# Optimization experiments

Measured on AMD Instinct MI355X. Metric: run time of the kernel, lower is better.

The kernel has to match this reference:

```python
import jax, jax.numpy as jnp
import numpy as np

EMBED_DIM = 384
NUM_HEADS = 6
HEAD_DIM = EMBED_DIM // NUM_HEADS
SCALE = HEAD_DIM ** (-0.5)
B, T, N = 8, 64, 196


def setup_inputs() -> dict:
    key = jax.random.key(0)
    k1, k2, k3, k4, k5 = jax.random.split(key, 5)
    x = jax.random.normal(k1, (B, T, N, EMBED_DIM), dtype=jnp.float32)
    W_qkv = jax.random.normal(k2, (3 * EMBED_DIM, EMBED_DIM), dtype=jnp.float32) * 0.02
    b_qkv = jax.random.normal(k3, (3 * EMBED_DIM,), dtype=jnp.float32) * 0.02
    W_proj = jax.random.normal(k4, (EMBED_DIM, EMBED_DIM), dtype=jnp.float32) * 0.02
    b_proj = jax.random.normal(k5, (EMBED_DIM,), dtype=jnp.float32) * 0.02
    return {"x": x, "W_qkv": W_qkv, "b_qkv": b_qkv, "W_proj": W_proj, "b_proj": b_proj}


def reference(x, W_qkv, b_qkv, W_proj, b_proj):
    b, t, n, c = x.shape
    # qkv projection: [B,T,N,3C] -> [B,T,N,3,H,hd] -> [3,B,H,T,N,hd]
    qkv = jnp.einsum('btnc,oc->btno', x, W_qkv) + b_qkv
    qkv = qkv.reshape(b, t, n, 3, NUM_HEADS, HEAD_DIM)
    qkv = jnp.transpose(qkv, (3, 0, 4, 1, 2, 5))
    q, k, v = qkv[0], qkv[1], qkv[2]
    q = q * SCALE
    # scores over patches within each block: [B,H,T,N,N]
    attn = jnp.einsum('bhtnd,bhtmd->bhtnm', q, k)
    attn = jax.nn.softmax(attn, axis=-1)
    out = jnp.einsum('bhtnm,bhtmd->bhtnd', attn, v)  # [B,H,T,N,hd]
    # Faithful to original: permute(0,2,3,4,1) puts head_dim before head, then flatten
    out = jnp.transpose(out, (0, 2, 3, 4, 1)).reshape(b, t, n, c)
    out = jnp.einsum('btnc,oc->btno', out, W_proj) + b_proj
    return out
```

## Files before the change

### kernel.cpp

```cpp
#include <hip/hip_runtime.h>
#include <cstdint>
#include <cstddef>

typedef unsigned short u16;
typedef __attribute__((ext_vector_type(4))) float f32x4;
typedef __attribute__((ext_vector_type(8))) __bf16 bf16x8;
typedef __attribute__((ext_vector_type(8))) unsigned short u16x8;
typedef __attribute__((ext_vector_type(4))) unsigned short u16x4;

#define M_TOTAL 100352
#define K_DIM   384
#define QKV_N   1152
#define NHEADS  6
#define NPAT    196
#define SCL     0.125f

__device__ __forceinline__ u16 f2bf(float f) {
    unsigned int u = __builtin_bit_cast(unsigned int, f);
    u += 0x7fffu + ((u >> 16) & 1u);
    return (u16)(u >> 16);
}

__device__ __forceinline__ void gload16(const void* g, void* l) {
    __builtin_amdgcn_global_load_lds(
        (const __attribute__((address_space(1))) unsigned int*)g,
        (__attribute__((address_space(3))) unsigned int*)l, 16, 0, 0);
}

__device__ __forceinline__ int xcd_swz(int bid, int per_xcd) {
    return (bid & 7) * per_xcd + (bid >> 3);
}

__global__ void cvt_bf16_kern(const float* __restrict__ in, u16* __restrict__ out, int n8) {
    int i = blockIdx.x * 256 + threadIdx.x;
    if (i >= n8) return;
    const float4* p = (const float4*)in + (size_t)i * 2;
    float4 a = p[0], b = p[1];
    u16x8 o;
    o[0]=f2bf(a.x); o[1]=f2bf(a.y); o[2]=f2bf(a.z); o[3]=f2bf(a.w);
    o[4]=f2bf(b.x); o[5]=f2bf(b.y); o[6]=f2bf(b.z); o[7]=f2bf(b.w);
    *((u16x8*)out + i) = o;
}

__global__ void cvt_wproj_kern(const float* __restrict__ in, u16* __restrict__ out) {
    int i = blockIdx.x * 256 + threadIdx.x;
    int o = i / 384;
    int c = i - o * 384;
    int d = c & 63, h = c >> 6;
    out[i] = f2bf(in[(size_t)o * 384 + d * 6 + h]);
}

template<int NOUT, bool BF16OUT, bool QSCALE>
__global__ __launch_bounds__(256, 2) void gemm_kern(
        const u16* __restrict__ A, const u16* __restrict__ Bw,
        const float* __restrict__ bias, void* __restrict__ outp) {
    constexpr int NB = NOUT / 128;
    constexpr int PER_XCD = (M_TOTAL / 128) * NB / 8;
    __shared__ u16 As[128 * 64];
    __shared__ u16 Bs[128 * 64];
    int wg = xcd_swz(blockIdx.x, PER_XCD);
    int bm = wg / NB, bn = wg % NB;
    int tid = threadIdx.x;
    int l = tid & 63, w = tid >> 6;
    int wr = w >> 1, wc = w & 1;
    f32x4 acc[4][4] = {};
    const u16* Ag = A + (size_t)bm * 128 * K_DIM;
    const u16* Bg = Bw + (size_t)bn * 128 * K_DIM;

    for (int ks = 0; ks < 6; ++ks) {
#pragma unroll
        for (int i = 0; i < 4; ++i) {
            int c = i * 256 + tid;
            int row = c >> 3, cc = c & 7;
            int scc = cc ^ (row & 7);
            gload16(Ag + (size_t)row * K_DIM + ks * 64 + scc * 8, (u16*)As + c * 8);
            gload16(Bg + (size_t)row * K_DIM + ks * 64 + scc * 8, (u16*)Bs + c * 8);
        }
        __syncthreads();
#pragma unroll
        for (int kk = 0; kk < 2; ++kk) {
            bf16x8 af[4], bfr[4];
            int ccr = kk * 4 + (l >> 4);
#pragma unroll
            for (int m = 0; m < 4; ++m) {
                int ar = wr * 64 + m * 16 + (l & 15);
                af[m] = *(const bf16x8*)&As[ar * 64 + ((ccr ^ (ar & 7)) << 3)];
            }
#pragma unroll
            for (int n = 0; n < 4; ++n) {
                int br = wc * 64 + n * 16 + (l & 15);
                bfr[n] = *(const bf16x8*)&Bs[br * 64 + ((ccr ^ (br & 7)) << 3)];
            }
#pragma unroll
            for (int m = 0; m < 4; ++m)
#pragma unroll
                for (int n = 0; n < 4; ++n)
                    acc[m][n] = __builtin_amdgcn_mfma_f32_16x16x32_bf16(af[m], bfr[n], acc[m][n], 0, 0, 0);
        }
        __syncthreads();
    }
#pragma unroll
    for (int n = 0; n < 4; ++n) {
        int col = bn * 128 + wc * 64 + n * 16 + (l & 15);
        float bv = bias[col];
#pragma unroll
        for (int m = 0; m < 4; ++m) {
            int row0 = bm * 128 + wr * 64 + m * 16 + (l >> 4) * 4;
#pragma unroll
            for (int r = 0; r < 4; ++r) {
                float v = acc[m][n][r] + bv;
                if constexpr (QSCALE) { if (col < 384) v *= SCL; }
                if constexpr (BF16OUT)
                    ((u16*)outp)[(size_t)(row0 + r) * NOUT + col] = f2bf(v);
                else
                    ((float*)outp)[(size_t)(row0 + r) * NOUT + col] = v;
            }
        }
    }
}

__global__ __launch_bounds__(256, 2) void attn_kern(const u16* __restrict__ qkv,
                                                    u16* __restrict__ osc) {
    __shared__ u16 k_lds[208 * 72];
    __shared__ u16 vT[64 * 232];
    __shared__ u16 p_lds[4 * 16 * 36];

    int wg = xcd_swz(blockIdx.x, 384);
    int h = wg % NHEADS;
    int bt = wg / NHEADS;
    size_t m_base = (size_t)bt * NPAT;
    int tid = threadIdx.x, l = tid & 63, w = tid >> 6;

    {
        int d0 = (tid & 7) * 8;
#pragma unroll
        for (int it = 0; it < 7; ++it) {
            int n = it * 32 + (tid >> 3);
            if (n < 208) {
                u16x8 val = {};
                if (n < 196)
                    val = *(const u16x8*)(qkv + (m_base + n) * QKV_N + 384 + h * 64 + d0);
                *(u16x8*)&k_lds[n * 72 + d0] = val;
            }
        }
    }
    {
        int d0 = w * 16;
#pragma unroll
        for (int it = 0; it < 4; ++it) {
            int n = it * 64 + l;
            if (n < 232) {
                u16x8 v0 = {}, v1 = {};
                if (n < 196) {
                    const u16* src = qkv + (m_base + n) * QKV_N + 768 + h * 64 + d0;
                    v0 = *(const u16x8*)src;
                    v1 = *(const u16x8*)(src + 8);
                }
#pragma unroll
                for (int j = 0; j < 8; ++j) {
                    vT[(d0 + j) * 232 + n] = v0[j];
                    vT[(d0 + 8 + j) * 232 + n] = v1[j];
                }
            }
        }
    }
    __syncthreads();

    u16* pw = &p_lds[w * 16 * 36];
    for (int qt = w; qt < 13; qt += 4) {
        int q0 = qt * 16;
        int qrow = q0 + (l & 15); if (qrow > 195) qrow = 195;
        const u16* qsrc = qkv + (m_base + qrow) * QKV_N + h * 64 + (l >> 4) * 8;
        bf16x8 aq0 = *(const bf16x8*)qsrc;
        bf16x8 aq1 = *(const bf16x8*)(qsrc + 32);

        f32x4 s[13];
#pragma unroll
        for (int f = 0; f < 13; ++f) {
            f32x4 a = {};
            bf16x8 b0 = *(const bf16x8*)&k_lds[(f * 16 + (l & 15)) * 72 + (l >> 4) * 8];
            a = __builtin_amdgcn_mfma_f32_16x16x32_bf16(aq0, b0, a, 0, 0, 0);
            bf16x8 b1 = *(const bf16x8*)&k_lds[(f * 16 + (l & 15)) * 72 + 32 + (l >> 4) * 8];
            a = __builtin_amdgcn_mfma_f32_16x16x32_bf16(aq1, b1, a, 0, 0, 0);
            s[f] = a;
        }
        float rs[4] = {0.f, 0.f, 0.f, 0.f};
#pragma unroll
        for (int f = 0; f < 13; ++f) {
#pragma unroll
            for (int r = 0; r < 4; ++r) {
                float e = __expf(s[f][r]);
                if (f == 12 && (l & 15) >= 4) e = 0.f;
                s[f][r] = e;
                rs[r] += e;
            }
        }
#pragma unroll
        for (int r = 0; r < 4; ++r) {
            float t = rs[r];
            t += __shfl_xor(t, 1);
            t += __shfl_xor(t, 2);
            t += __shfl_xor(t, 4);
            t += __shfl_xor(t, 8);
            rs[r] = __builtin_amdgcn_rcpf(t);
        }
        f32x4 o[4] = {};
#pragma unroll
        for (int kb = 0; kb < 7; ++kb) {
#pragma unroll
            for (int fh = 0; fh < 2; ++fh) {
                int f = kb * 2 + fh;
#pragma unroll
                for (int r = 0; r < 4; ++r) {
                    float pv = 0.f;
                    if (f < 13) pv = s[f][r];
                    pw[((l >> 4) * 4 + r) * 36 + fh * 16 + (l & 15)] = f2bf(pv);
                }
            }
            u16x4 lo = *(const u16x4*)&pw[(l & 15) * 36 + (l >> 4) * 8];
            u16x4 hi = *(const u16x4*)&pw[(l & 15) * 36 + (l >> 4) * 8 + 4];
            union { u16x4 h4[2]; bf16x8 v8; } uu;
            uu.h4[0] = lo; uu.h4[1] = hi;
            bf16x8 pa = uu.v8;
#pragma unroll
            for (int j = 0; j < 4; ++j) {
                bf16x8 bv = *(const bf16x8*)&vT[(j * 16 + (l & 15)) * 232 + kb * 32 + (l >> 4) * 8];
                o[j] = __builtin_amdgcn_mfma_f32_16x16x32_bf16(pa, bv, o[j], 0, 0, 0);
            }
        }
#pragma unroll
        for (int j = 0; j < 4; ++j) {
#pragma unroll
            for (int r = 0; r < 4; ++r) {
                int q = q0 + (l >> 4) * 4 + r;
                if (q < 196)
                    osc[(m_base + q) * 384 + h * 64 + j * 16 + (l & 15)] = f2bf(o[j][r] * rs[r]);
            }
        }
    }
}

extern "C" void kernel_launch(void* const* d_in, const int* in_sizes, int n_in,
                              void* d_out, int out_size, void* d_ws, size_t ws_size,
                              hipStream_t stream) {
    const float* x     = (const float*)d_in[0];
    const float* Wqkv  = (const float*)d_in[1];
    const float* bqkv  = (const float*)d_in[2];
    const float* Wproj = (const float*)d_in[3];
    const float* bproj = (const float*)d_in[4];

    const size_t need = ((size_t)M_TOTAL * 384 + (size_t)M_TOTAL * QKV_N
                         + (size_t)QKV_N * K_DIM + (size_t)K_DIM * K_DIM) * 2;
    if (ws_size < need) {
        hipMemsetAsync(d_out, 0, (size_t)out_size * 4, stream);
        return;
    }

    u16* xbf    = (u16*)d_ws;
    u16* qkvb   = xbf + (size_t)M_TOTAL * 384;
    u16* wqkvb  = qkvb + (size_t)M_TOTAL * QKV_N;
    u16* wprojb = wqkvb + (size_t)QKV_N * K_DIM;

    cvt_bf16_kern<<<18816, 256, 0, stream>>>(x, xbf, 4816896);
    cvt_bf16_kern<<<216, 256, 0, stream>>>(Wqkv, wqkvb, 55296);
    cvt_wproj_kern<<<576, 256, 0, stream>>>(Wproj, wprojb);

    gemm_kern<QKV_N, true, true><<<7056, 256, 0, stream>>>(xbf, wqkvb, bqkv, qkvb);
    attn_kern<<<3072, 256, 0, stream>>>(qkvb, xbf);
    gemm_kern<384, false, false><<<2352, 256, 0, stream>>>(xbf, wprojb, bproj, (float*)d_out);
}
```

Before: 354.5 us.

## Widen GEMM tile to 128x384 with 512 threads and double-buffered LDS

The GEMM kernel now uses 512-thread workgroups computing 128x384 output tiles, so each A tile is loaded once per 384 output columns instead of once per 128. It also double-buffers the A/B tiles in LDS, issuing the next k-step's global-to-LDS loads before computing the current one, with explicit vmcnt waits and barriers. The aim is to cut redundant A traffic and hide load latency. In exchange, LDS use grows to about 128 KB per block, which may limit occupancy, and accumulator register pressure rises to 24 tiles per wave.

```diff
diff --git a/kernel.cpp b/kernel.cpp
--- a/kernel.cpp
+++ b/kernel.cpp
@@ -51,57 +51,81 @@
 }
 
 template<int NOUT, bool BF16OUT, bool QSCALE>
-__global__ __launch_bounds__(256, 2) void gemm_kern(
+__global__ __launch_bounds__(512, 2) void gemm_kern(
         const u16* __restrict__ A, const u16* __restrict__ Bw,
         const float* __restrict__ bias, void* __restrict__ outp) {
-    constexpr int NB = NOUT / 128;
+    constexpr int BN = 384;
+    constexpr int NB = NOUT / BN;
+    constexpr int NREP = BN / 4 / 16;
     constexpr int PER_XCD = (M_TOTAL / 128) * NB / 8;
-    __shared__ u16 As[128 * 64];
-    __shared__ u16 Bs[128 * 64];
+    __shared__ __align__(16) u16 As[2][128 * 64];
+    __shared__ __align__(16) u16 Bs[2][BN * 64];
+
     int wg = xcd_swz(blockIdx.x, PER_XCD);
     int bm = wg / NB, bn = wg % NB;
     int tid = threadIdx.x;
     int l = tid & 63, w = tid >> 6;
-    int wr = w >> 1, wc = w & 1;
-    f32x4 acc[4][4] = {};
+    int wr = w >> 2, wc = w & 3;
     const u16* Ag = A + (size_t)bm * 128 * K_DIM;
-    const u16* Bg = Bw + (size_t)bn * 128 * K_DIM;
-
+    const u16* Bg = Bw + (size_t)bn * BN * K_DIM;
+
+    auto stage = [&](int buf, int ks) {
+        const u16* ag = Ag + ks * 64;
+#pragma unroll
+        for (int i = 0; i < 2; ++i) {
+            int c = i * 512 + tid;
+            int row = c >> 3, cc = c & 7, scc = cc ^ (row & 7);
+            gload16(ag + (size_t)row * K_DIM + scc * 8, (u16*)As[buf] + c * 8);
+        }
+        const u16* bg = Bg + ks * 64;
+#pragma unroll
+        for (int i = 0; i < 6; ++i) {
+            int c = i * 512 + tid;
+            int row = c >> 3, cc = c & 7, scc = cc ^ (row & 7);
+            gload16(bg + (size_t)row * K_DIM + scc * 8, (u16*)Bs[buf] + c * 8);
+        }
+    };
+
+    f32x4 acc[4][NREP] = {};
+    stage(0, 0);
     for (int ks = 0; ks < 6; ++ks) {
-#pragma unroll
-        for (int i = 0; i < 4; ++i) {
-            int c = i * 256 + tid;
-            int row = c >> 3, cc = c & 7;
-            int scc = cc ^ (row & 7);
-            gload16(Ag + (size_t)row * K_DIM + ks * 64 + scc * 8, (u16*)As + c * 8);
-            gload16(Bg + (size_t)row * K_DIM + ks * 64 + scc * 8, (u16*)Bs + c * 8);
-        }
-        __syncthreads();
+        int cur = ks & 1;
+        if (ks < 5) {
+            stage(cur ^ 1, ks + 1);
+            asm volatile("s_waitcnt vmcnt(8)" ::: "memory");
+        } else {
+            asm volatile("s_waitcnt vmcnt(0)" ::: "memory");
+        }
+        __builtin_amdgcn_sched_barrier(0);
+        __builtin_amdgcn_s_barrier();
+        __builtin_amdgcn_sched_barrier(0);
 #pragma unroll
         for (int kk = 0; kk < 2; ++kk) {
-            bf16x8 af[4], bfr[4];
             int ccr = kk * 4 + (l >> 4);
+            bf16x8 af[4], bfr[NREP];
 #pragma unroll
             for (int m = 0; m < 4; ++m) {
                 int ar = wr * 64 + m * 16 + (l & 15);
-                af[m] = *(const bf16x8*)&As[ar * 64 + ((ccr ^ (ar & 7)) << 3)];
-            }
-#pragma unroll
-            for (int n = 0; n < 4; ++n) {
-                int br = wc * 64 + n * 16 + (l & 15);
-                bfr[n] = *(const bf16x8*)&Bs[br * 64 + ((ccr ^ (br & 7)) << 3)];
+                af[m] = *(const bf16x8*)&As[cur][ar * 64 + ((ccr ^ (ar & 7)) << 3)];
+            }
+#pragma unroll
+            for (int n = 0; n < NREP; ++n) {
+                int br = wc * 96 + n * 16 + (l & 15);
+                bfr[n] = *(const bf16x8*)&Bs[cur][br * 64 + ((ccr ^ (br & 7)) << 3)];
             }
 #pragma unroll
             for (int m = 0; m < 4; ++m)
 #pragma unroll
-                for (int n = 0; n < 4; ++n)
+                for (int n = 0; n < NREP; ++n)
                     acc[m][n] = __builtin_amdgcn_mfma_f32_16x16x32_bf16(af[m], bfr[n], acc[m][n], 0, 0, 0);
         }
-        __syncthreads();
-    }
-#pragma unroll
-    for (int n = 0; n < 4; ++n) {
-        int col = bn * 128 + wc * 64 + n * 16 + (l & 15);
+        __builtin_amdgcn_sched_barrier(0);
+        __builtin_amdgcn_s_barrier();
+        __builtin_amdgcn_sched_barrier(0);
+    }
+#pragma unroll
+    for (int n = 0; n < NREP; ++n) {
+        int col = bn * BN + wc * 96 + n * 16 + (l & 15);
         float bv = bias[col];
 #pragma unroll
         for (int m = 0; m < 4; ++m) {
@@ -265,7 +289,7 @@
     cvt_bf16_kern<<<216, 256, 0, stream>>>(Wqkv, wqkvb, 55296);
     cvt_wproj_kern<<<576, 256, 0, stream>>>(Wproj, wprojb);
 
-    gemm_kern<QKV_N, true, true><<<7056, 256, 0, stream>>>(xbf, wqkvb, bqkv, qkvb);
+    gemm_kern<QKV_N, true, true><<<2352, 512, 0, stream>>>(xbf, wqkvb, bqkv, qkvb);
     attn_kern<<<3072, 256, 0, stream>>>(qkvb, xbf);
-    gemm_kern<384, false, false><<<2352, 256, 0, stream>>>(xbf, wprojb, bproj, (float*)d_out);
-}
+    gemm_kern<384, false, false><<<784, 512, 0, stream>>>(xbf, wprojb, bproj, (float*)d_out);
+}
```

New measurement: 393.8 us. +11.1%, slower.

## Compute transposed scores and feed P to PV MFMA directly from registers

Applied to the files above, without the earlier changes.

Swaps the MFMA operands in the QK^T step so each lane holds score columns for one query row, and permutes the K rows in LDS so the score fragment layout matches the A-operand layout of the PV MFMA. The probabilities are normalized, packed to bf16 pairs in registers and fed straight into the PV MFMAs. This removes the per-wave LDS round trip for P and the 16-lane shuffle reductions. It costs extra registers for the packed P arrays and relies on the permuted K layout being exactly consistent with the MFMA fragment mapping.

```diff
diff --git a/kernel.cpp b/kernel.cpp
--- a/kernel.cpp
+++ b/kernel.cpp
@@ -6,7 +6,6 @@
 typedef __attribute__((ext_vector_type(4))) float f32x4;
 typedef __attribute__((ext_vector_type(8))) __bf16 bf16x8;
 typedef __attribute__((ext_vector_type(8))) unsigned short u16x8;
-typedef __attribute__((ext_vector_type(4))) unsigned short u16x4;
 
 #define M_TOTAL 100352
 #define K_DIM   384
@@ -19,6 +18,12 @@
     unsigned int u = __builtin_bit_cast(unsigned int, f);
     u += 0x7fffu + ((u >> 16) & 1u);
     return (u16)(u >> 16);
+}
+
+__device__ __forceinline__ unsigned int pack2(float a, float b) {
+    union { __bf16 h[2]; unsigned int u; } p;
+    p.h[0] = (__bf16)a; p.h[1] = (__bf16)b;
+    return p.u;
 }
 
 __device__ __forceinline__ void gload16(const void* g, void* l) {
@@ -121,27 +126,26 @@
 
 __global__ __launch_bounds__(256, 2) void attn_kern(const u16* __restrict__ qkv,
                                                     u16* __restrict__ osc) {
-    __shared__ u16 k_lds[208 * 72];
+    __shared__ u16 k_lds[224 * 72];
     __shared__ u16 vT[64 * 232];
-    __shared__ u16 p_lds[4 * 16 * 36];
 
     int wg = xcd_swz(blockIdx.x, 384);
     int h = wg % NHEADS;
     int bt = wg / NHEADS;
     size_t m_base = (size_t)bt * NPAT;
     int tid = threadIdx.x, l = tid & 63, w = tid >> 6;
+    int lr = l & 15, lg = l >> 4;
 
     {
         int d0 = (tid & 7) * 8;
 #pragma unroll
         for (int it = 0; it < 7; ++it) {
             int n = it * 32 + (tid >> 3);
-            if (n < 208) {
-                u16x8 val = {};
-                if (n < 196)
-                    val = *(const u16x8*)(qkv + (m_base + n) * QKV_N + 384 + h * 64 + d0);
-                *(u16x8*)&k_lds[n * 72 + d0] = val;
-            }
+            u16x8 val = {};
+            if (n < 196)
+                val = *(const u16x8*)(qkv + (m_base + n) * QKV_N + 384 + h * 64 + d0);
+            int pr = (2 * (n >> 5) + ((n >> 2) & 1)) * 16 + ((n >> 3) & 3) * 4 + (n & 3);
+            *(u16x8*)&k_lds[pr * 72 + d0] = val;
         }
     }
     {
@@ -166,75 +170,64 @@
     }
     __syncthreads();
 
-    u16* pw = &p_lds[w * 16 * 36];
     for (int qt = w; qt < 13; qt += 4) {
         int q0 = qt * 16;
-        int qrow = q0 + (l & 15); if (qrow > 195) qrow = 195;
-        const u16* qsrc = qkv + (m_base + qrow) * QKV_N + h * 64 + (l >> 4) * 8;
-        bf16x8 aq0 = *(const bf16x8*)qsrc;
-        bf16x8 aq1 = *(const bf16x8*)(qsrc + 32);
+        int qrow = q0 + lr; if (qrow > 195) qrow = 195;
+        const u16* qsrc = qkv + (m_base + qrow) * QKV_N + h * 64 + lg * 8;
+        bf16x8 bq0 = *(const bf16x8*)qsrc;
+        bf16x8 bq1 = *(const bf16x8*)(qsrc + 32);
 
         f32x4 s[13];
 #pragma unroll
         for (int f = 0; f < 13; ++f) {
             f32x4 a = {};
-            bf16x8 b0 = *(const bf16x8*)&k_lds[(f * 16 + (l & 15)) * 72 + (l >> 4) * 8];
-            a = __builtin_amdgcn_mfma_f32_16x16x32_bf16(aq0, b0, a, 0, 0, 0);
-            bf16x8 b1 = *(const bf16x8*)&k_lds[(f * 16 + (l & 15)) * 72 + 32 + (l >> 4) * 8];
-            a = __builtin_amdgcn_mfma_f32_16x16x32_bf16(aq1, b1, a, 0, 0, 0);
+            bf16x8 k0 = *(const bf16x8*)&k_lds[(f * 16 + lr) * 72 + lg * 8];
+            a = __builtin_amdgcn_mfma_f32_16x16x32_bf16(k0, bq0, a, 0, 0, 0);
+            bf16x8 k1 = *(const bf16x8*)&k_lds[(f * 16 + lr) * 72 + 32 + lg * 8];
+            a = __builtin_amdgcn_mfma_f32_16x16x32_bf16(k1, bq1, a, 0, 0, 0);
             s[f] = a;
         }
-        float rs[4] = {0.f, 0.f, 0.f, 0.f};
-#pragma unroll
-        for (int f = 0; f < 13; ++f) {
+        float sum = 0.f;
+#pragma unroll
+        for (int f = 0; f < 13; ++f)
 #pragma unroll
             for (int r = 0; r < 4; ++r) {
                 float e = __expf(s[f][r]);
-                if (f == 12 && (l & 15) >= 4) e = 0.f;
+                if (f == 12 && lg > 0) e = 0.f;
                 s[f][r] = e;
-                rs[r] += e;
-            }
-        }
-#pragma unroll
-        for (int r = 0; r < 4; ++r) {
-            float t = rs[r];
-            t += __shfl_xor(t, 1);
-            t += __shfl_xor(t, 2);
-            t += __shfl_xor(t, 4);
-            t += __shfl_xor(t, 8);
-            rs[r] = __builtin_amdgcn_rcpf(t);
-        }
+                sum += e;
+            }
+        sum += __shfl_xor(sum, 16);
+        sum += __shfl_xor(sum, 32);
+        float rs = __builtin_amdgcn_rcpf(sum);
+
+        unsigned int pk0[14], pk1[14];
+#pragma unroll
+        for (int f = 0; f < 13; ++f) {
+            pk0[f] = pack2(s[f][0] * rs, s[f][1] * rs);
+            pk1[f] = pack2(s[f][2] * rs, s[f][3] * rs);
+        }
+        pk0[13] = 0u; pk1[13] = 0u;
+
         f32x4 o[4] = {};
 #pragma unroll
         for (int kb = 0; kb < 7; ++kb) {
-#pragma unroll
-            for (int fh = 0; fh < 2; ++fh) {
-                int f = kb * 2 + fh;
-#pragma unroll
-                for (int r = 0; r < 4; ++r) {
-                    float pv = 0.f;
-                    if (f < 13) pv = s[f][r];
-                    pw[((l >> 4) * 4 + r) * 36 + fh * 16 + (l & 15)] = f2bf(pv);
-                }
-            }
-            u16x4 lo = *(const u16x4*)&pw[(l & 15) * 36 + (l >> 4) * 8];
-            u16x4 hi = *(const u16x4*)&pw[(l & 15) * 36 + (l >> 4) * 8 + 4];
-            union { u16x4 h4[2]; bf16x8 v8; } uu;
-            uu.h4[0] = lo; uu.h4[1] = hi;
-            bf16x8 pa = uu.v8;
+            union { unsigned int u[4]; bf16x8 v; } pa;
+            pa.u[0] = pk0[2 * kb];     pa.u[1] = pk1[2 * kb];
+            pa.u[2] = pk0[2 * kb + 1]; pa.u[3] = pk1[2 * kb + 1];
 #pragma unroll
             for (int j = 0; j < 4; ++j) {
-                bf16x8 bv = *(const bf16x8*)&vT[(j * 16 + (l & 15)) * 232 + kb * 32 + (l >> 4) * 8];
-                o[j] = __builtin_amdgcn_mfma_f32_16x16x32_bf16(pa, bv, o[j], 0, 0, 0);
+                bf16x8 bv = *(const bf16x8*)&vT[(j * 16 + lr) * 232 + kb * 32 + lg * 8];
+                o[j] = __builtin_amdgcn_mfma_f32_16x16x32_bf16(pa.v, bv, o[j], 0, 0, 0);
             }
         }
 #pragma unroll
         for (int j = 0; j < 4; ++j) {
 #pragma unroll
             for (int r = 0; r < 4; ++r) {
-                int q = q0 + (l >> 4) * 4 + r;
+                int q = q0 + lg * 4 + r;
                 if (q < 196)
-                    osc[(m_base + q) * 384 + h * 64 + j * 16 + (l & 15)] = f2bf(o[j][r] * rs[r]);
+                    osc[(m_base + q) * 384 + h * 64 + j * 16 + lr] = f2bf(o[j][r]);
             }
         }
     }
```

Measured after the change: 450.9 us. 27.2% more time.
